# Kernel optimization log

Hardware: AMD Instinct MI355X
Metric: run time of the kernel (lower is better)

Reference implementation:

```python
import jax, jax.numpy as jnp
import numpy as np

QUERY_LEVELS = jnp.array([300, 500, 900, 1500], dtype=jnp.int32)
MAX_K = 1500
NUM_BOUNDARIES = 3
MAX_OBJECTS = 1500
SCALE = MAX_OBJECTS / NUM_BOUNDARIES * 0.3  # 150.0


def _layernorm(x, g, b, eps=1e-5):
    m = jnp.mean(x, axis=-1, keepdims=True)
    v = jnp.var(x, axis=-1, keepdims=True)
    return (x - m) * jax.lax.rsqrt(v + eps) * g + b


def setup_inputs() -> dict:
    key = jax.random.key(0)
    ks = jax.random.split(key, 14)
    B, C, H, W = 8, 256, 100, 100
    s = 0.02
    return {
        "density_feature": jax.random.normal(ks[0], (B, C, H, W), jnp.float32),
        "encoder_features": jax.random.normal(ks[1], (B, C, H, W), jnp.float32),
        # input_norm (LayerNorm over 2*C)
        "ln_in_g": jnp.ones((2 * C,), jnp.float32),
        "ln_in_b": jnp.zeros((2 * C,), jnp.float32),
        # fc_boundary: Linear(2C->C), Linear(C->3)
        "fcb_w1": jax.random.normal(ks[2], (C, 2 * C), jnp.float32) * s,
        "fcb_b1": jnp.zeros((C,), jnp.float32),
        "fcb_w2": jax.random.normal(ks[3], (NUM_BOUNDARIES, C), jnp.float32) * s,
        "fcb_b2": jnp.full((NUM_BOUNDARIES,), -3.0, jnp.float32),
        "cr_ln_g": jnp.ones((C,), jnp.float32),
        "cr_ln_b": jnp.zeros((C,), jnp.float32),
        "cr_w1": jax.random.normal(ks[4], (C, C), jnp.float32) * s,
        "cr_b1": jnp.zeros((C,), jnp.float32),
        "cr_w2": jax.random.normal(ks[5], (1, C), jnp.float32) * s,
        "cr_b2": jnp.full((1,), 4.0, jnp.float32),
        # channel attention 1x1 convs: C->C//16->C
        "ca_w1": jax.random.normal(ks[6], (C // 16, C), jnp.float32) * s,
        "ca_b1": jnp.zeros((C // 16,), jnp.float32),
        "ca_w2": jax.random.normal(ks[7], (C, C // 16), jnp.float32) * s,
        "ca_b2": jnp.zeros((C,), jnp.float32),
        # spatial attention 7x7 conv, 2->1, no bias
        "sa_w": jax.random.normal(ks[8], (1, 2, 7, 7), jnp.float32) * s,
        # spatial_weight_conv 1x1, C->1
        "sw_w": jax.random.normal(ks[9], (1, C), jnp.float32) * s,
        "sw_b": jnp.zeros((1,), jnp.float32),
    }


def reference(density_feature, encoder_features, ln_in_g, ln_in_b,
              fcb_w1, fcb_b1, fcb_w2, fcb_b2,
              cr_ln_g, cr_ln_b, cr_w1, cr_b1, cr_w2, cr_b2,
              ca_w1, ca_b1, ca_w2, ca_b2, sa_w, sw_w, sw_b):
    B, C, H, W = density_feature.shape
    df = jnp.clip(density_feature, -5.0, 5.0)
    ef = jnp.clip(encoder_features, -5.0, 5.0)

    # ---- boundary prediction from density feature ----
    feat_avg = jnp.mean(df, axis=(2, 3))            # [B, C]
    feat_max = jnp.max(df, axis=(2, 3))             # [B, C]
    gfeat = jnp.concatenate([feat_avg, feat_max], axis=1)  # [B, 2C]
    gfeat = _layernorm(gfeat, ln_in_g, ln_in_b)
    h = jax.nn.relu(gfeat @ fcb_w1.T + fcb_b1)
    raw_boundaries = h @ fcb_w2.T + fcb_b2           # [B, 3]
    # cumulative: b_i = sum_{j<=i} (softplus(raw_j)*SCALE + 5)
    boundaries = jnp.cumsum(jax.nn.softplus(raw_boundaries) * SCALE + 5.0, axis=1)

    cr = _layernorm(feat_avg, cr_ln_g, cr_ln_b)
    cr = jax.nn.relu(cr @ cr_w1.T + cr_b1)
    pred_count = jax.nn.softplus(cr @ cr_w2.T + cr_b2)[:, 0]  # [B]

    # ---- num_queries via boundary comparison (eval: N_eval = pred_count) ----
    level = ((pred_count > boundaries[:, 0]).astype(jnp.int32)
             + (pred_count > boundaries[:, 1]).astype(jnp.int32)
             + (pred_count > boundaries[:, 2]).astype(jnp.int32))
    num_queries = QUERY_LEVELS[level]

    # ---- CBAM channel attention ----
    x = ef
    gap = jnp.mean(x, axis=(2, 3))                   # [B, C]
    ca = jax.nn.relu(gap @ ca_w1.T + ca_b1)
    ca = jax.nn.sigmoid(ca @ ca_w2.T + ca_b2)        # [B, C]
    x = x * ca[:, :, None, None]

    # ---- CBAM spatial attention ----
    sa_avg = jnp.mean(x, axis=1, keepdims=True)      # [B,1,H,W]
    sa_max = jnp.max(x, axis=1, keepdims=True)
    sa = jnp.concatenate([sa_avg, sa_max], axis=1)   # [B,2,H,W]
    sa = jax.lax.conv_general_dilated(sa, sa_w, (1, 1), [(3, 3), (3, 3)],
                                      dimension_numbers=("NCHW", "OIHW", "NCHW"))
    x = x * jax.nn.sigmoid(sa)

    # ---- spatial weight map + topk reference points ----
    wmap = jax.nn.sigmoid(jnp.einsum("bchw,oc->bohw", x, sw_w) + sw_b[None, :, None, None])
    spatial_weight_map = wmap.reshape(B, 1, H * W)
    weight_flat = wmap.reshape(B, H * W)
    actual_k = min(H * W, MAX_K)
    _, topk_ind = jax.lax.top_k(weight_flat, actual_k)   # [B, k]
    topk_y = ((topk_ind // W).astype(jnp.float32) + 0.5) / H
    topk_x = ((topk_ind % W).astype(jnp.float32) + 0.5) / W
    ref_points = jnp.stack([topk_x, topk_y], axis=-1)    # [B,k,2]
    ref_points = jnp.concatenate([ref_points, jnp.full_like(ref_points, 0.05)], axis=-1)
    if actual_k < MAX_K:
        pad = jnp.zeros((B, MAX_K - actual_k, 4), ref_points.dtype)
        ref_points = jnp.concatenate([ref_points, pad], axis=1)

    return (boundaries, raw_boundaries, pred_count, num_queries,
            spatial_weight_map, ref_points)
```

## Files before the change

kernel.cpp:

```cpp
#include <hip/hip_runtime.h>
#include <cstdint>
#include <cstddef>

#define BB 8
#define CC 256
#define HH 100
#define WW 100
#define HW 10000
#define KTOP 1500

#define WS_AVG   0
#define WS_MAX   2048
#define WS_GAP   4096
#define WS_CA    6144
#define WS_CASW  8192
#define WS_SW    10240
#define WS_SAVG  90240
#define WS_SMAX  170240

#define O_BND 0
#define O_RAW 24
#define O_CNT 48
#define O_NQ  56
#define O_WMAP 64
#define O_REF 80064

__device__ __forceinline__ float clip5(float v){ return fminf(fmaxf(v, -5.f), 5.f); }
__device__ __forceinline__ float softplusf(float x){ return fmaxf(x, 0.f) + log1pf(expf(-fabsf(x))); }
__device__ __forceinline__ float sigmoidf(float x){ return 1.f / (1.f + expf(-x)); }

__device__ __forceinline__ float wsum(float v){
#pragma unroll
  for (int o = 32; o; o >>= 1) v += __shfl_down(v, o, 64);
  return v;
}
__device__ __forceinline__ float wmaxr(float v){
#pragma unroll
  for (int o = 32; o; o >>= 1) v = fmaxf(v, __shfl_down(v, o, 64));
  return v;
}

__device__ __forceinline__ float bsum256(float v, volatile float* red){
  v = wsum(v);
  int w = threadIdx.x >> 6;
  if ((threadIdx.x & 63) == 0) red[w] = v;
  __syncthreads();
  float r = (red[0] + red[1]) + (red[2] + red[3]);
  __syncthreads();
  return r;
}

__global__ __launch_bounds__(256) void k_reduce(const float* __restrict__ df,
                                                const float* __restrict__ ef,
                                                float* __restrict__ ws){
  int blk = blockIdx.x;
  bool isDf = blk < 2048;
  int bc = isDf ? blk : blk - 2048;
  const float4* src = reinterpret_cast<const float4*>((isDf ? df : ef) + (size_t)bc * HW);
  float s = 0.f, m = -1e30f;
  for (int i = threadIdx.x; i < HW / 4; i += 256){
    float4 v = src[i];
    float a = clip5(v.x), b = clip5(v.y), c = clip5(v.z), d = clip5(v.w);
    s += (a + b) + (c + d);
    m = fmaxf(m, fmaxf(fmaxf(a, b), fmaxf(c, d)));
  }
  __shared__ float rs[4], rm[4];
  s = wsum(s); m = wmaxr(m);
  int w = threadIdx.x >> 6;
  if ((threadIdx.x & 63) == 0){ rs[w] = s; rm[w] = m; }
  __syncthreads();
  if (threadIdx.x == 0){
    float S = (rs[0] + rs[1]) + (rs[2] + rs[3]);
    float M = fmaxf(fmaxf(rm[0], rm[1]), fmaxf(rm[2], rm[3]));
    if (isDf){ ws[WS_AVG + bc] = S * (1.f / HW); ws[WS_MAX + bc] = M; }
    else      { ws[WS_GAP + bc] = S * (1.f / HW); }
  }
}

__global__ __launch_bounds__(256) void k_head(float* __restrict__ ws,
    const float* __restrict__ ln_g, const float* __restrict__ ln_b,
    const float* __restrict__ fw1, const float* __restrict__ fb1,
    const float* __restrict__ fw2, const float* __restrict__ fb2,
    const float* __restrict__ crg, const float* __restrict__ crb,
    const float* __restrict__ cw1, const float* __restrict__ cb1,
    const float* __restrict__ cw2, const float* __restrict__ cb2,
    const float* __restrict__ caw1, const float* __restrict__ cab1,
    const float* __restrict__ caw2, const float* __restrict__ cab2,
    const float* __restrict__ sw_w, float* __restrict__ out){
  int b = blockIdx.x, t = threadIdx.x;
  __shared__ float red[4];
  __shared__ float gl[512];
  __shared__ float hl[256];
  __shared__ float rawl[3];
  __shared__ float bnd[3];
  __shared__ float al[16];

  float fa = ws[WS_AVG + b * CC + t];
  float fm = ws[WS_MAX + b * CC + t];

  float s  = bsum256(fa + fm, red);
  float s2 = bsum256(fa * fa + fm * fm, red);
  float mean = s * (1.f / 512.f);
  float var  = s2 * (1.f / 512.f) - mean * mean;
  float inv  = rsqrtf(var + 1e-5f);
  gl[t]       = (fa - mean) * inv * ln_g[t]       + ln_b[t];
  gl[t + 256] = (fm - mean) * inv * ln_g[t + 256] + ln_b[t + 256];
  __syncthreads();

  float acc = fb1[t];
#pragma unroll 8
  for (int k = 0; k < 512; k++) acc += gl[k] * fw1[t * 512 + k];
  hl[t] = fmaxf(acc, 0.f);
  __syncthreads();
  if (t < 3){
    float r = fb2[t];
    for (int j = 0; j < 256; j++) r += hl[j] * fw2[t * 256 + j];
    rawl[t] = r;
  }
  __syncthreads();
  if (t == 0){
    float cum = 0.f;
    for (int o = 0; o < 3; o++){
      float rv = rawl[o];
      out[O_RAW + b * 3 + o] = rv;
      cum += softplusf(rv) * 150.f + 5.f;
      out[O_BND + b * 3 + o] = cum;
      bnd[o] = cum;
    }
  }
  __syncthreads();

  float sc  = bsum256(fa, red);
  float sc2 = bsum256(fa * fa, red);
  float m2 = sc * (1.f / 256.f);
  float v2 = sc2 * (1.f / 256.f) - m2 * m2;
  float inv2 = rsqrtf(v2 + 1e-5f);
  hl[t] = (fa - m2) * inv2 * crg[t] + crb[t];
  __syncthreads();
  float acc2 = cb1[t];
#pragma unroll 8
  for (int k = 0; k < 256; k++) acc2 += hl[k] * cw1[t * 256 + k];
  float h2 = fmaxf(acc2, 0.f);
  float pv = bsum256(h2 * cw2[t], red);
  if (t == 0){
    float pred = softplusf(pv + cb2[0]);
    out[O_CNT + b] = pred;
    int lvl = (pred > bnd[0]) + (pred > bnd[1]) + (pred > bnd[2]);
    const float QL[4] = {300.f, 500.f, 900.f, 1500.f};
    out[O_NQ + b] = QL[lvl];
  }

  float gp = ws[WS_GAP + b * CC + t];
  __syncthreads();
  hl[t] = gp;
  __syncthreads();
  if (t < 16){
    float a = cab1[t];
    for (int k = 0; k < 256; k++) a += hl[k] * caw1[t * 256 + k];
    al[t] = fmaxf(a, 0.f);
  }
  __syncthreads();
  float a2 = cab2[t];
#pragma unroll
  for (int k = 0; k < 16; k++) a2 += al[k] * caw2[t * 16 + k];
  float cav = sigmoidf(a2);
  ws[WS_CA + b * CC + t]   = cav;
  ws[WS_CASW + b * CC + t] = cav * sw_w[t];
}

__global__ __launch_bounds__(256) void k_pixel(const float* __restrict__ ef,
                                               float* __restrict__ ws){
  int b = blockIdx.y;
  int p = blockIdx.x * 256 + threadIdx.x;
  __shared__ float caL[256], cswL[256];
  caL[threadIdx.x]  = ws[WS_CA + b * CC + threadIdx.x];
  cswL[threadIdx.x] = ws[WS_CASW + b * CC + threadIdx.x];
  __syncthreads();
  if (p >= HW) return;
  const float* base = ef + (size_t)b * CC * HW + p;
  float sum = 0.f, mx = -1e30f, sw = 0.f;
#pragma unroll 4
  for (int c = 0; c < CC; c++){
    float v = clip5(base[(size_t)c * HW]);
    float x = v * caL[c];
    sum += x;
    mx = fmaxf(mx, x);
    sw = fmaf(v, cswL[c], sw);
  }
  ws[WS_SAVG + b * HW + p] = sum * (1.f / 256.f);
  ws[WS_SMAX + b * HW + p] = mx;
  ws[WS_SW + b * HW + p]   = sw;
}

__global__ __launch_bounds__(256) void k_conv(const float* __restrict__ ws,
                                              const float* __restrict__ sa_w,
                                              const float* __restrict__ sw_b,
                                              float* __restrict__ out){
  __shared__ float wc[98];
  if (threadIdx.x < 98) wc[threadIdx.x] = sa_w[threadIdx.x];
  __syncthreads();
  int b = blockIdx.y;
  int p = blockIdx.x * 256 + threadIdx.x;
  if (p >= HW) return;
  int h = p / WW, w = p - h * WW;
  const float* s0 = ws + WS_SAVG + (size_t)b * HW;
  const float* s1 = ws + WS_SMAX + (size_t)b * HW;
  float acc = 0.f;
#pragma unroll
  for (int kh = 0; kh < 7; kh++){
    int hy = h + kh - 3;
    if (hy < 0 || hy >= HH) continue;
#pragma unroll
    for (int kw = 0; kw < 7; kw++){
      int wx = w + kw - 3;
      if (wx < 0 || wx >= WW) continue;
      int q = hy * WW + wx;
      acc += s0[q] * wc[kh * 7 + kw] + s1[q] * wc[49 + kh * 7 + kw];
    }
  }
  float wm = sigmoidf(ws[WS_SW + (size_t)b * HW + p] * sigmoidf(acc) + sw_b[0]);
  out[O_WMAP + (size_t)b * HW + p] = wm;
}

__global__ __launch_bounds__(1024) void k_select(const float* __restrict__ outw,
                                                 float* __restrict__ out){
  __shared__ unsigned vals[HW];
  __shared__ unsigned long long AKl[KTOP];
  __shared__ unsigned red32[16];
  __shared__ unsigned sbc;
  __shared__ unsigned acnt, runbase;
  int b = blockIdx.x, t = threadIdx.x;
  int w = t >> 6, lane = t & 63;

  const float* src = outw + O_WMAP + (size_t)b * HW;
  unsigned rv[10];
#pragma unroll
  for (int j = 0; j < 10; j++){
    int i = t + j * 1024;
    unsigned v = (i < HW) ? __float_as_uint(src[i]) : 0u;
    rv[j] = v;
    if (i < HW) vals[i] = v;
  }
  __syncthreads();

  unsigned lo = 0u, hi = 0xFFFFFFFFu;
  while (lo < hi){
    unsigned mid = lo + ((hi - lo) >> 1);
    unsigned c = 0;
#pragma unroll
    for (int j = 0; j < 10; j++) c += (rv[j] > mid) ? 1u : 0u;
#pragma unroll
    for (int o = 32; o; o >>= 1) c += __shfl_down((int)c, o, 64);
    if (lane == 0) red32[w] = c;
    __syncthreads();
    if (t == 0){
      unsigned tot = 0;
#pragma unroll
      for (int q = 0; q < 16; q++) tot += red32[q];
      sbc = tot;
    }
    __syncthreads();
    unsigned cnt = sbc;
    if (cnt < (unsigned)KTOP) hi = mid; else lo = mid + 1u;
  }
  unsigned vthr = lo;

  {
    unsigned c = 0;
#pragma unroll
    for (int j = 0; j < 10; j++) c += (rv[j] > vthr) ? 1u : 0u;
#pragma unroll
    for (int o = 32; o; o >>= 1) c += __shfl_down((int)c, o, 64);
    if (lane == 0) red32[w] = c;
    __syncthreads();
    if (t == 0){
      unsigned tot = 0;
#pragma unroll
      for (int q = 0; q < 16; q++) tot += red32[q];
      sbc = tot;
      acnt = 0; runbase = 0;
    }
    __syncthreads();
  }
  unsigned nabove = sbc;
  int neq = KTOP - (int)nabove;

#pragma unroll
  for (int j = 0; j < 10; j++){
    int i = t + j * 1024;
    if (i < HW && rv[j] > vthr){
      unsigned pos = atomicAdd(&acnt, 1u);
      AKl[pos] = ((unsigned long long)rv[j] << 32) | (unsigned long long)(0xFFFFFFFFu - (unsigned)i);
    }
  }

  for (int i0 = 0; i0 < HW; i0 += 1024){
    int i = i0 + t;
    unsigned v = (i < HW) ? vals[i] : 0u;
    bool eq = (i < HW) && (v == vthr);
    unsigned long long bal = __ballot(eq);
    if (lane == 0) red32[w] = (unsigned)__popcll(bal);
    __syncthreads();
    unsigned pre = runbase;
    for (int q = 0; q < w; q++) pre += red32[q];
    unsigned myr = pre + (unsigned)__popcll(bal & ((1ull << lane) - 1ull));
    if (eq && myr < (unsigned)neq){
      int pos = (int)nabove + (int)myr;
      float y = ((float)(i / WW) + 0.5f) * (1.f / HH);
      float x = ((float)(i % WW) + 0.5f) * (1.f / WW);
      float* rp = out + O_REF + ((size_t)b * KTOP + pos) * 4;
      rp[0] = x; rp[1] = y; rp[2] = 0.05f; rp[3] = 0.05f;
    }
    __syncthreads();
    if (t == 0){
      unsigned tot = 0;
#pragma unroll
      for (int q = 0; q < 16; q++) tot += red32[q];
      runbase += tot;
    }
    __syncthreads();
  }

  int nA = (int)nabove;
  for (int i = t; i < nA; i += 1024){
    unsigned long long Ki = AKl[i];
    int r = 0;
    for (int j = 0; j < nA; j++) r += (AKl[j] > Ki) ? 1 : 0;
    unsigned idx = 0xFFFFFFFFu - (unsigned)(Ki & 0xFFFFFFFFull);
    float y = ((float)(idx / WW) + 0.5f) * (1.f / HH);
    float x = ((float)(idx % WW) + 0.5f) * (1.f / WW);
    float* rp = out + O_REF + ((size_t)b * KTOP + r) * 4;
    rp[0] = x; rp[1] = y; rp[2] = 0.05f; rp[3] = 0.05f;
  }
}

extern "C" void kernel_launch(void* const* d_in, const int* in_sizes, int n_in,
                              void* d_out, int out_size, void* d_ws, size_t ws_size,
                              hipStream_t stream) {
  const float* df   = (const float*)d_in[0];
  const float* ef   = (const float*)d_in[1];
  const float* ln_g = (const float*)d_in[2];
  const float* ln_b = (const float*)d_in[3];
  const float* fw1  = (const float*)d_in[4];
  const float* fb1  = (const float*)d_in[5];
  const float* fw2  = (const float*)d_in[6];
  const float* fb2  = (const float*)d_in[7];
  const float* crg  = (const float*)d_in[8];
  const float* crb  = (const float*)d_in[9];
  const float* cw1  = (const float*)d_in[10];
  const float* cb1  = (const float*)d_in[11];
  const float* cw2  = (const float*)d_in[12];
  const float* cb2  = (const float*)d_in[13];
  const float* caw1 = (const float*)d_in[14];
  const float* cab1 = (const float*)d_in[15];
  const float* caw2 = (const float*)d_in[16];
  const float* cab2 = (const float*)d_in[17];
  const float* sa_w = (const float*)d_in[18];
  const float* sw_w = (const float*)d_in[19];
  const float* sw_b = (const float*)d_in[20];
  float* out = (float*)d_out;
  float* ws  = (float*)d_ws;

  k_reduce<<<4096, 256, 0, stream>>>(df, ef, ws);
  k_head<<<8, 256, 0, stream>>>(ws, ln_g, ln_b, fw1, fb1, fw2, fb2,
                                crg, crb, cw1, cb1, cw2, cb2,
                                caw1, cab1, caw2, cab2, sw_w, out);
  k_pixel<<<dim3(40, 8), 256, 0, stream>>>(ef, ws);
  k_conv<<<dim3(40, 8), 256, 0, stream>>>(ws, sa_w, sw_b, out);
  k_select<<<8, 1024, 0, stream>>>(out, out);
}
```

Measured before the change: 178.7 us.

## Split top-k ranking into separate kernel and use 4-way threshold search

Top-k selection now uses a quaternary search over the float bit threshold, packing three counts into one 64-bit reduction, which halves the number of block-wide barrier rounds. Above-threshold keys go to workspace through wave-aggregated atomics, and the equal-value scan stops early once enough ties are found. The O(n^2) rank sort moves out of the 8-block select kernel into a new 96-block kernel so the quadratic work spreads over more CUs. The cost is an extra launch plus a workspace round trip for the keys.

```diff
diff --git a/kernel.cpp b/kernel.cpp
--- a/kernel.cpp
+++ b/kernel.cpp
@@ -17,6 +17,8 @@
 #define WS_SW    10240
 #define WS_SAVG  90240
 #define WS_SMAX  170240
+#define WS_SEL   250240
+#define WS_AK    250248
 
 #define O_BND 0
 #define O_RAW 24
@@ -223,11 +225,11 @@
 }
 
 __global__ __launch_bounds__(1024) void k_select(const float* __restrict__ outw,
+                                                 float* __restrict__ ws,
                                                  float* __restrict__ out){
-  __shared__ unsigned vals[HW];
-  __shared__ unsigned long long AKl[KTOP];
+  __shared__ unsigned long long red64[16];
   __shared__ unsigned red32[16];
-  __shared__ unsigned sbc;
+  __shared__ unsigned slo, shi, sbc;
   __shared__ unsigned acnt, runbase;
   int b = blockIdx.x, t = threadIdx.x;
   int w = t >> 6, lane = t & 63;
@@ -237,31 +239,44 @@
 #pragma unroll
   for (int j = 0; j < 10; j++){
     int i = t + j * 1024;
-    unsigned v = (i < HW) ? __float_as_uint(src[i]) : 0u;
-    rv[j] = v;
-    if (i < HW) vals[i] = v;
-  }
-  __syncthreads();
+    rv[j] = (i < HW) ? __float_as_uint(src[i]) : 0u;
+  }
 
   unsigned lo = 0u, hi = 0xFFFFFFFFu;
   while (lo < hi){
-    unsigned mid = lo + ((hi - lo) >> 1);
-    unsigned c = 0;
-#pragma unroll
-    for (int j = 0; j < 10; j++) c += (rv[j] > mid) ? 1u : 0u;
-#pragma unroll
-    for (int o = 32; o; o >>= 1) c += __shfl_down((int)c, o, 64);
-    if (lane == 0) red32[w] = c;
+    unsigned span = hi - lo;
+    unsigned q1 = lo + (span >> 2);
+    unsigned q2 = lo + (span >> 1);
+    unsigned q3 = lo + span - (span >> 2);
+    unsigned long long pk = 0;
+#pragma unroll
+    for (int j = 0; j < 10; j++){
+      unsigned v = rv[j];
+      pk += (unsigned long long)(v > q1)
+          + ((unsigned long long)(v > q2) << 16)
+          + ((unsigned long long)(v > q3) << 32);
+    }
+#pragma unroll
+    for (int o = 32; o; o >>= 1) pk += __shfl_down(pk, o, 64);
+    if (lane == 0) red64[w] = pk;
     __syncthreads();
     if (t == 0){
-      unsigned tot = 0;
-#pragma unroll
-      for (int q = 0; q < 16; q++) tot += red32[q];
-      sbc = tot;
-    }
-    __syncthreads();
-    unsigned cnt = sbc;
-    if (cnt < (unsigned)KTOP) hi = mid; else lo = mid + 1u;
+      unsigned long long tot = 0;
+#pragma unroll
+      for (int q = 0; q < 16; q++) tot += red64[q];
+      unsigned c1 = (unsigned)(tot & 0xFFFFu);
+      unsigned c2 = (unsigned)((tot >> 16) & 0xFFFFu);
+      unsigned c3 = (unsigned)((tot >> 32) & 0xFFFFu);
+      unsigned nlo, nhi;
+      if (c1 < (unsigned)KTOP)      { nlo = lo;      nhi = q1; }
+      else if (c2 < (unsigned)KTOP) { nlo = q1 + 1u; nhi = q2; }
+      else if (c3 < (unsigned)KTOP) { nlo = q2 + 1u; nhi = q3; }
+      else                          { nlo = q3 + 1u; nhi = hi; }
+      slo = nlo; shi = nhi;
+    }
+    __syncthreads();
+    lo = slo; hi = shi;
+    __syncthreads();
   }
   unsigned vthr = lo;
 
@@ -284,20 +299,26 @@
   }
   unsigned nabove = sbc;
   int neq = KTOP - (int)nabove;
-
+  if (t == 0) reinterpret_cast<int*>(ws)[WS_SEL + b] = (int)nabove;
+
+  unsigned long long* AK = reinterpret_cast<unsigned long long*>(ws + WS_AK) + (size_t)b * KTOP;
 #pragma unroll
   for (int j = 0; j < 10; j++){
     int i = t + j * 1024;
-    if (i < HW && rv[j] > vthr){
-      unsigned pos = atomicAdd(&acnt, 1u);
-      AKl[pos] = ((unsigned long long)rv[j] << 32) | (unsigned long long)(0xFFFFFFFFu - (unsigned)i);
-    }
-  }
-
-  for (int i0 = 0; i0 < HW; i0 += 1024){
-    int i = i0 + t;
-    unsigned v = (i < HW) ? vals[i] : 0u;
-    bool eq = (i < HW) && (v == vthr);
+    bool p = (i < HW) && (rv[j] > vthr);
+    unsigned long long m = __ballot(p);
+    unsigned base = 0;
+    if (lane == 0 && m) base = atomicAdd(&acnt, (unsigned)__popcll(m));
+    base = (unsigned)__shfl((int)base, 0, 64);
+    if (p){
+      unsigned pos = base + (unsigned)__popcll(m & ((1ull << lane) - 1ull));
+      AK[pos] = ((unsigned long long)rv[j] << 32) | (unsigned long long)(0xFFFFFFFFu - (unsigned)i);
+    }
+  }
+
+  for (int j = 0; j < 10; j++){
+    int i = j * 1024 + t;
+    bool eq = (i < HW) && (rv[j] == vthr);
     unsigned long long bal = __ballot(eq);
     if (lane == 0) red32[w] = (unsigned)__popcll(bal);
     __syncthreads();
@@ -319,19 +340,29 @@
       runbase += tot;
     }
     __syncthreads();
-  }
-
-  int nA = (int)nabove;
-  for (int i = t; i < nA; i += 1024){
-    unsigned long long Ki = AKl[i];
-    int r = 0;
-    for (int j = 0; j < nA; j++) r += (AKl[j] > Ki) ? 1 : 0;
-    unsigned idx = 0xFFFFFFFFu - (unsigned)(Ki & 0xFFFFFFFFull);
-    float y = ((float)(idx / WW) + 0.5f) * (1.f / HH);
-    float x = ((float)(idx % WW) + 0.5f) * (1.f / WW);
-    float* rp = out + O_REF + ((size_t)b * KTOP + r) * 4;
-    rp[0] = x; rp[1] = y; rp[2] = 0.05f; rp[3] = 0.05f;
-  }
+    if (runbase >= (unsigned)neq) break;
+  }
+}
+
+__global__ __launch_bounds__(128) void k_rank(const float* __restrict__ ws,
+                                              float* __restrict__ out){
+  int b = blockIdx.x, chunk = blockIdx.y, t = threadIdx.x;
+  int nA = reinterpret_cast<const int*>(ws)[WS_SEL + b];
+  __shared__ unsigned long long K[KTOP];
+  const unsigned long long* AK =
+      reinterpret_cast<const unsigned long long*>(ws + WS_AK) + (size_t)b * KTOP;
+  for (int i = t; i < nA; i += 128) K[i] = AK[i];
+  __syncthreads();
+  int i = chunk * 128 + t;
+  if (i >= nA) return;
+  unsigned long long Ki = K[i];
+  int r = 0;
+  for (int j = 0; j < nA; j++) r += (K[j] > Ki);
+  unsigned idx = 0xFFFFFFFFu - (unsigned)(Ki & 0xFFFFFFFFull);
+  float y = ((float)(idx / WW) + 0.5f) * (1.f / HH);
+  float x = ((float)(idx % WW) + 0.5f) * (1.f / WW);
+  float* rp = out + O_REF + ((size_t)b * KTOP + r) * 4;
+  rp[0] = x; rp[1] = y; rp[2] = 0.05f; rp[3] = 0.05f;
 }
 
 extern "C" void kernel_launch(void* const* d_in, const int* in_sizes, int n_in,
@@ -367,5 +398,6 @@
                                 caw1, cab1, caw2, cab2, sw_w, out);
   k_pixel<<<dim3(40, 8), 256, 0, stream>>>(ef, ws);
   k_conv<<<dim3(40, 8), 256, 0, stream>>>(ws, sa_w, sw_b, out);
-  k_select<<<8, 1024, 0, stream>>>(out, out);
-}
+  k_select<<<8, 1024, 0, stream>>>(out, ws, out);
+  k_rank<<<dim3(8, 12), 128, 0, stream>>>(ws, out);
+}
```

Result: faster. 162.8 us (-8.9%).
